# Performance work log

Hardware: AMD Instinct MI355X
Metric: run time of the kernel (lower is better)

Reference implementation:

```python
import jax, jax.numpy as jnp
import numpy as np

N_WIRES = 25                    # odd -> RX on wire 0, then SingleExcitation on (1,2),(3,4),...,(23,24)
DIM = 2 ** N_WIRES              # 33_554_432 amplitudes
N_THETA = (N_WIRES + 1) // 2    # 13


def _apply_rx(state, th, wire):
    """Apply RX(th) = [[cos, -i sin], [-i sin, cos]] (half-angle) to `wire`.
    PennyLane convention: wire 0 is the most-significant bit of the amplitude index."""
    c = jnp.cos(th * 0.5)
    ms = -1j * jnp.sin(th * 0.5)
    st = state.reshape(2 ** wire, 2, -1)          # [pre, 2, post]
    s0, s1 = st[:, 0], st[:, 1]
    new = jnp.stack([c * s0 + ms * s1, ms * s0 + c * s1], axis=1)
    return new.reshape(-1)


def _apply_single_excitation(state, phi, wire):
    """SingleExcitation(phi) on wires [wire, wire+1]: rotates the |01>,|10> subspace
    by angle phi/2; |00>,|11> untouched."""
    c = jnp.cos(phi * 0.5)
    s = jnp.sin(phi * 0.5)
    st = state.reshape(2 ** wire, 2, 2, -1)       # [pre, q_i, q_{i+1}, post]
    a00, a01, a10, a11 = st[:, 0, 0], st[:, 0, 1], st[:, 1, 0], st[:, 1, 1]
    n01 = c * a01 - s * a10
    n10 = s * a01 + c * a10
    new = jnp.stack([jnp.stack([a00, n01], axis=1),
                     jnp.stack([n10, a11], axis=1)], axis=1)
    return new.reshape(-1)


def setup_inputs() -> dict:
    key = jax.random.key(0)
    kf, kt = jax.random.split(key)
    feature = jax.random.normal(kf, (DIM,), dtype=jnp.float32)
    # he_normal init on shape (13, 1): std = sqrt(2 / fan_in) with fan_in = 13
    theta = jax.random.normal(kt, (N_THETA, 1), dtype=jnp.float32) * np.sqrt(2.0 / N_THETA)
    return {"feature": feature, "theta": theta}


def reference(feature, theta) -> jnp.ndarray:
    # AmplitudeEmbedding with pad_with=0.0: pad (no-op here, len == 2^n) then L2-normalize
    state = (feature / jnp.linalg.norm(feature)).astype(jnp.complex64)
    # odd wire count: RX(theta[0][0]) on wire 0, start pair gates at wire 1
    state = _apply_rx(state, theta[0, 0], 0)
    for i in range(1, N_WIRES, 2):                # i = 1,3,...,23 -> theta[0..11]
        state = _apply_single_excitation(state, theta[i // 2, 0], i)
    return jnp.real(state)
```

## Files before the change

### kernel.cpp

```cpp
#include <hip/hip_runtime.h>
#include <math.h>


typedef float f32x4 __attribute__((ext_vector_type(4)));

static __device__ __forceinline__ float4 nt_load4(const float* p) {
    f32x4 v = __builtin_nontemporal_load((const f32x4*)p);
    return *(float4*)&v;
}
static __device__ __forceinline__ void nt_store4(float* p, float4 v) {
    __builtin_nontemporal_store(*(f32x4*)&v, (f32x4*)p);
}

static __device__ __forceinline__ void bar_lgkm() {
    asm volatile("s_waitcnt lgkmcnt(0)\n\ts_barrier" ::: "memory");
}

static __device__ __forceinline__ void rot4(float4& a, float4& b, float c, float s) {
    float4 na, nb;
    na.x = c*a.x - s*b.x;  nb.x = s*a.x + c*b.x;
    na.y = c*a.y - s*b.y;  nb.y = s*a.y + c*b.y;
    na.z = c*a.z - s*b.z;  nb.z = s*a.z + c*b.z;
    na.w = c*a.w - s*b.w;  nb.w = s*a.w + c*b.w;
    a = na; b = nb;
}

static __device__ __forceinline__ float4 shflx4(float4 v, int m) {
    float4 r;
    r.x = __shfl_xor(v.x, m, 64);
    r.y = __shfl_xor(v.y, m, 64);
    r.z = __shfl_xor(v.z, m, 64);
    r.w = __shfl_xor(v.w, m, 64);
    return r;
}

template <int NR>
static __device__ __forceinline__ void rotshfl(float4* f, int sh, float c, float s, int lane) {
    const int pv = (lane >> sh) & 3;
    const bool act = (pv == 1) || (pv == 2);
    const float cl = act ? c : 1.0f;
    const float sl = act ? ((pv == 1) ? -s : s) : 0.0f;
    const int m = 3 << sh;
#pragma unroll
    for (int k = 0; k < NR; ++k) {
        float4 p = shflx4(f[k], m);
        float4 n;
        n.x = fmaf(sl, p.x, cl * f[k].x);
        n.y = fmaf(sl, p.y, cl * f[k].y);
        n.z = fmaf(sl, p.z, cl * f[k].z);
        n.w = fmaf(sl, p.w, cl * f[k].w);
        f[k] = n;
    }
}

static __device__ __forceinline__ float sumsq16(const float4* f) {
    float q[16];
#pragma unroll
    for (int k = 0; k < 16; ++k)
        q[k] = fmaf(f[k].x, f[k].x,
               fmaf(f[k].y, f[k].y,
               fmaf(f[k].z, f[k].z, f[k].w * f[k].w)));
#pragma unroll
    for (int st = 1; st < 16; st <<= 1)
#pragma unroll
        for (int i = 0; i < 16; i += (st << 1))
            q[i] += q[i + st];
    return q[0];
}

__global__ __launch_bounds__(256, 2) void qnn_p1(const float* __restrict__ in,
                                                 const float* __restrict__ theta,
                                                 float* __restrict__ out,
                                                 double* __restrict__ partials) {
    __shared__ __align__(16) float4 lds[4096];
    __shared__ double red[4];
    const int t = threadIdx.x, lane = t & 63, w2 = t >> 6;
    const long gA = (long)blockIdx.x << 13;
    const long gB = gA + 4096;

    float c0,s0,c1,s1,c2,s2,c3,s3,c4,s4,c5,s5,c6,s6;
    { float th;
      th=0.5f*theta[11]; c0=cosf(th); s0=sinf(th);
      th=0.5f*theta[10]; c1=cosf(th); s1=sinf(th);
      th=0.5f*theta[9];  c2=cosf(th); s2=sinf(th);
      th=0.5f*theta[8];  c3=cosf(th); s3=sinf(th);
      th=0.5f*theta[7];  c4=cosf(th); s4=sinf(th);
      th=0.5f*theta[6];  c5=cosf(th); s5=sinf(th);
      th=0.5f*theta[5];  c6=cosf(th); s6=sinf(th); }

    float4 f[16], g[16];
#pragma unroll
    for (int k = 0; k < 16; ++k)
        f[k] = nt_load4(in + ((gA + ((w2 << 10) | (k << 6) | lane)) << 2));
#pragma unroll
    for (int k = 0; k < 16; ++k)
        g[k] = nt_load4(in + ((gB + ((w2 << 10) | (k << 6) | lane)) << 2));

    const float sA = sumsq16(f);

#pragma unroll
    for (int k = 0; k < 16; ++k) {
        float ny = c0*f[k].y - s0*f[k].z;
        float nz = s0*f[k].y + c0*f[k].z;
        f[k].y = ny; f[k].z = nz;
    }
    rotshfl<16>(f, 0, c1, s1, lane);
    rotshfl<16>(f, 2, c2, s2, lane);
    rotshfl<16>(f, 4, c3, s3, lane);
#pragma unroll
    for (int hi = 0; hi < 16; hi += 4) rot4(f[hi+1], f[hi+2], c4, s4);
#pragma unroll
    for (int lo = 0; lo < 4; ++lo)     rot4(f[4+lo], f[8+lo], c5, s5);

#pragma unroll
    for (int k = 0; k < 16; ++k) lds[(w2 << 10) | (k << 6) | lane] = f[k];
    bar_lgkm();
#pragma unroll
    for (int m = 0; m < 16; ++m) f[m] = lds[(m << 8) | (w2 << 6) | lane];
#pragma unroll
    for (int lo = 0; lo < 4; ++lo) rot4(f[4+lo], f[8+lo], c6, s6);
#pragma unroll
    for (int m = 0; m < 16; ++m)
        *(float4*)(out + ((gA + ((m << 8) | (w2 << 6) | lane)) << 2)) = f[m];

    const float sB = sumsq16(g);
#pragma unroll
    for (int k = 0; k < 16; ++k) {
        float ny = c0*g[k].y - s0*g[k].z;
        float nz = s0*g[k].y + c0*g[k].z;
        g[k].y = ny; g[k].z = nz;
    }
    rotshfl<16>(g, 0, c1, s1, lane);
    rotshfl<16>(g, 2, c2, s2, lane);
    rotshfl<16>(g, 4, c3, s3, lane);
#pragma unroll
    for (int hi = 0; hi < 16; hi += 4) rot4(g[hi+1], g[hi+2], c4, s4);
#pragma unroll
    for (int lo = 0; lo < 4; ++lo)     rot4(g[4+lo], g[8+lo], c5, s5);

    bar_lgkm();
#pragma unroll
    for (int k = 0; k < 16; ++k) lds[(w2 << 10) | (k << 6) | lane] = g[k];
    bar_lgkm();
#pragma unroll
    for (int m = 0; m < 16; ++m) g[m] = lds[(m << 8) | (w2 << 6) | lane];
#pragma unroll
    for (int lo = 0; lo < 4; ++lo) rot4(g[4+lo], g[8+lo], c6, s6);
#pragma unroll
    for (int m = 0; m < 16; ++m)
        *(float4*)(out + ((gB + ((m << 8) | (w2 << 6) | lane)) << 2)) = g[m];

    double acc = (double)sA + (double)sB;
#pragma unroll
    for (int off = 32; off > 0; off >>= 1) acc += __shfl_down(acc, off, 64);
    if (lane == 0) red[w2] = acc;
    bar_lgkm();
    if (t == 0)
        partials[blockIdx.x] = red[0] + red[1] + red[2] + red[3];
}

__global__ void qnn_norm(const double* __restrict__ partials,
                         const float* __restrict__ theta,
                         double* __restrict__ scale) {
    __shared__ double w[4];
    const int t = threadIdx.x;
    double acc = 0.0;
    for (int i = t; i < 1024; i += 256) acc += partials[i];
#pragma unroll
    for (int off = 32; off > 0; off >>= 1) acc += __shfl_down(acc, off, 64);
    if ((t & 63) == 0) w[t >> 6] = acc;
    __syncthreads();
    if (t == 0) {
        double tot = w[0] + w[1] + w[2] + w[3];
        *scale = (double)cosf(0.5f * theta[0]) / sqrt(tot);
    }
}

__global__ __launch_bounds__(512, 2) void qnn_high(float* __restrict__ buf,
                                                   const float* __restrict__ theta,
                                                   const double* __restrict__ scale) {
    __shared__ __align__(16) float4 lds[8192];
    const int t = threadIdx.x, lane = t & 63;
    const int bid = blockIdx.x;
    const int b24 = bid >> 8, mid = bid & 255;
    const long baseA = ((long)b24 << 22) | ((long)mid << 4);
    const long baseB = baseA | (1L << 21);

    float c7,s7,c8,s8,c9,s9,c10,s10,c11,s11;
    { float th;
      th=0.5f*theta[4]; c7 =cosf(th); s7 =sinf(th);
      th=0.5f*theta[3]; c8 =cosf(th); s8 =sinf(th);
      th=0.5f*theta[2]; c9 =cosf(th); s9 =sinf(th);
      th=0.5f*theta[1]; c10=cosf(th); s10=sinf(th);
      th=0.5f*theta[0]; c11=cosf(th); s11=sinf(th); }
    const float sc = (float)(*scale);

    float4 f[16], g[16];
#pragma unroll
    for (int k = 0; k < 16; ++k) {
        const int s_ = (k << 9) | t;
        f[k] = *(const float4*)(buf + ((baseA | ((long)(s_ >> 4) << 12) | (s_ & 15)) << 2));
    }
#pragma unroll
    for (int k = 0; k < 16; ++k) {
        const int s_ = (k << 9) | t;
        g[k] = *(const float4*)(buf + ((baseB | ((long)(s_ >> 4) << 12) | (s_ & 15)) << 2));
    }

    rotshfl<16>(f, 4, c7, s7, lane);
    rotshfl<16>(g, 4, c7, s7, lane);
#pragma unroll
    for (int h8 = 0; h8 < 16; h8 += 8) {
        rot4(f[h8+2], f[h8+4], c10, s10);
        rot4(f[h8+3], f[h8+5], c10, s10);
        rot4(g[h8+2], g[h8+4], c10, s10);
        rot4(g[h8+3], g[h8+5], c10, s10);
    }
#pragma unroll
    for (int i = 0; i < 8; ++i)
        rot4(f[8+i], g[i], c11, s11);

#pragma unroll
    for (int k = 0; k < 16; ++k) lds[(k << 9) | t] = f[k];
    bar_lgkm();
    {
        const int rb = ((t >> 6) << 10) | (t & 63);
#pragma unroll
        for (int m = 0; m < 16; ++m) f[m] = lds[rb | (m << 6)];
#pragma unroll
        for (int q = 0; q < 16; q += 4) rot4(f[q+1], f[q+2], c8, s8);
#pragma unroll
        for (int lo = 0; lo < 4; ++lo)  rot4(f[4+lo], f[8+lo], c9, s9);
#pragma unroll
        for (int m = 0; m < 16; ++m) {
            const int s_ = rb | (m << 6);
            float4 v = f[m];
            v.x *= sc; v.y *= sc; v.z *= sc; v.w *= sc;
            nt_store4(buf + ((baseA | ((long)(s_ >> 4) << 12) | (s_ & 15)) << 2), v);
        }
    }
    bar_lgkm();

#pragma unroll
    for (int k = 0; k < 16; ++k) lds[(k << 9) | t] = g[k];
    bar_lgkm();
    {
        const int rb = ((t >> 6) << 10) | (t & 63);
#pragma unroll
        for (int m = 0; m < 16; ++m) g[m] = lds[rb | (m << 6)];
#pragma unroll
        for (int q = 0; q < 16; q += 4) rot4(g[q+1], g[q+2], c8, s8);
#pragma unroll
        for (int lo = 0; lo < 4; ++lo)  rot4(g[4+lo], g[8+lo], c9, s9);
#pragma unroll
        for (int m = 0; m < 16; ++m) {
            const int s_ = rb | (m << 6);
            float4 v = g[m];
            v.x *= sc; v.y *= sc; v.z *= sc; v.w *= sc;
            nt_store4(buf + ((baseB | ((long)(s_ >> 4) << 12) | (s_ & 15)) << 2), v);
        }
    }
}

extern "C" void kernel_launch(void* const* d_in, const int* in_sizes, int n_in,
                              void* d_out, int out_size, void* d_ws, size_t ws_size,
                              hipStream_t stream) {
    const float* in = (const float*)d_in[0];
    const float* theta = (const float*)d_in[1];
    float* out = (float*)d_out;
    double* part = (double*)d_ws;
    double* scale = part + 1024;

    qnn_p1<<<1024, 256, 0, stream>>>(in, theta, out, part);
    qnn_norm<<<1, 256, 0, stream>>>(part, theta, scale);
    qnn_high<<<512, 512, 0, stream>>>(out, theta, scale);
}
```

Baseline: 93.53 us.

## Move theta[4] gate into first pass and rebalance bit-to-pass mapping

Changes which index bits each block of the first pass holds, so the gate on bits 12-13 (theta[4]) is applied there by pairing the A and B tiles, removing the shuffle-based rotation from the second pass. The second pass gets a new address mapping with 32-element contiguous runs in place of 16, so each global access segment is longer. The cost is a data-dependent branch in the first pass and only half the blocks doing the extra rotation, which creates some imbalance between blocks.

```diff
diff --git a/kernel.cpp b/kernel.cpp
--- a/kernel.cpp
+++ b/kernel.cpp
@@ -75,10 +75,12 @@
     __shared__ __align__(16) float4 lds[4096];
     __shared__ double red[4];
     const int t = threadIdx.x, lane = t & 63, w2 = t >> 6;
-    const long gA = (long)blockIdx.x << 13;
-    const long gB = gA + 4096;
-
-    float c0,s0,c1,s1,c2,s2,c3,s3,c4,s4,c5,s5,c6,s6;
+    const int bid = blockIdx.x;
+    const int h = bid >> 1, p = bid & 1;
+    const long gA = ((long)h << 14) | (p ? (1L << 12) : 0);
+    const long gB = ((long)h << 14) | (p ? (2L << 12) : (3L << 12));
+
+    float c0,s0,c1,s1,c2,s2,c3,s3,c4,s4,c5,s5,c6,s6,c7,s7;
     { float th;
       th=0.5f*theta[11]; c0=cosf(th); s0=sinf(th);
       th=0.5f*theta[10]; c1=cosf(th); s1=sinf(th);
@@ -86,7 +88,8 @@
       th=0.5f*theta[8];  c3=cosf(th); s3=sinf(th);
       th=0.5f*theta[7];  c4=cosf(th); s4=sinf(th);
       th=0.5f*theta[6];  c5=cosf(th); s5=sinf(th);
-      th=0.5f*theta[5];  c6=cosf(th); s6=sinf(th); }
+      th=0.5f*theta[5];  c6=cosf(th); s6=sinf(th);
+      th=0.5f*theta[4];  c7=cosf(th); s7=sinf(th); }
 
     float4 f[16], g[16];
 #pragma unroll
@@ -97,6 +100,12 @@
         g[k] = nt_load4(in + ((gB + ((w2 << 10) | (k << 6) | lane)) << 2));
 
     const float sA = sumsq16(f);
+    const float sB = sumsq16(g);
+
+    if (p) {
+#pragma unroll
+        for (int k = 0; k < 16; ++k) rot4(f[k], g[k], c7, s7);
+    }
 
 #pragma unroll
     for (int k = 0; k < 16; ++k) {
@@ -123,7 +132,6 @@
     for (int m = 0; m < 16; ++m)
         *(float4*)(out + ((gA + ((m << 8) | (w2 << 6) | lane)) << 2)) = f[m];
 
-    const float sB = sumsq16(g);
 #pragma unroll
     for (int k = 0; k < 16; ++k) {
         float ny = c0*g[k].y - s0*g[k].z;
@@ -156,7 +164,7 @@
     if (lane == 0) red[w2] = acc;
     bar_lgkm();
     if (t == 0)
-        partials[blockIdx.x] = red[0] + red[1] + red[2] + red[3];
+        partials[bid] = red[0] + red[1] + red[2] + red[3];
 }
 
 __global__ void qnn_norm(const double* __restrict__ partials,
@@ -180,85 +188,78 @@
                                                    const float* __restrict__ theta,
                                                    const double* __restrict__ scale) {
     __shared__ __align__(16) float4 lds[8192];
-    const int t = threadIdx.x, lane = t & 63;
+    const int t = threadIdx.x;
     const int bid = blockIdx.x;
-    const int b24 = bid >> 8, mid = bid & 255;
-    const long baseA = ((long)b24 << 22) | ((long)mid << 4);
-    const long baseB = baseA | (1L << 21);
-
-    float c7,s7,c8,s8,c9,s9,c10,s10,c11,s11;
+    const int f1514 = bid >> 7, mid = bid & 127;
+    const long gqA = ((long)f1514 << 12) | ((long)mid << 5);
+    const long gqB = gqA | (1L << 22);
+
+    float c8,s8,c9,s9,c10,s10,c11,s11;
     { float th;
-      th=0.5f*theta[4]; c7 =cosf(th); s7 =sinf(th);
       th=0.5f*theta[3]; c8 =cosf(th); s8 =sinf(th);
       th=0.5f*theta[2]; c9 =cosf(th); s9 =sinf(th);
       th=0.5f*theta[1]; c10=cosf(th); s10=sinf(th);
       th=0.5f*theta[0]; c11=cosf(th); s11=sinf(th); }
     const float sc = (float)(*scale);
 
+    const int rb = ((t >> 5) << 9) | (t & 31);
+
     float4 f[16], g[16];
 #pragma unroll
     for (int k = 0; k < 16; ++k) {
         const int s_ = (k << 9) | t;
-        f[k] = *(const float4*)(buf + ((baseA | ((long)(s_ >> 4) << 12) | (s_ & 15)) << 2));
+        f[k] = *(const float4*)(buf + ((gqA | ((long)(s_ >> 5) << 14) | (s_ & 31)) << 2));
     }
 #pragma unroll
     for (int k = 0; k < 16; ++k) {
         const int s_ = (k << 9) | t;
-        g[k] = *(const float4*)(buf + ((baseB | ((long)(s_ >> 4) << 12) | (s_ & 15)) << 2));
-    }
-
-    rotshfl<16>(f, 4, c7, s7, lane);
-    rotshfl<16>(g, 4, c7, s7, lane);
-#pragma unroll
-    for (int h8 = 0; h8 < 16; h8 += 8) {
-        rot4(f[h8+2], f[h8+4], c10, s10);
-        rot4(f[h8+3], f[h8+5], c10, s10);
-        rot4(g[h8+2], g[h8+4], c10, s10);
-        rot4(g[h8+3], g[h8+5], c10, s10);
-    }
-#pragma unroll
-    for (int i = 0; i < 8; ++i)
-        rot4(f[8+i], g[i], c11, s11);
+        g[k] = *(const float4*)(buf + ((gqB | ((long)(s_ >> 5) << 14) | (s_ & 31)) << 2));
+    }
+
+#pragma unroll
+    for (int q = 0; q < 16; q += 4) {
+        rot4(f[q+1], f[q+2], c10, s10);
+        rot4(g[q+1], g[q+2], c10, s10);
+    }
+#pragma unroll
+    for (int lo = 0; lo < 4; ++lo) {
+        rot4(f[4+lo], f[8+lo], c11, s11);
+        rot4(g[4+lo], g[8+lo], c11, s11);
+    }
 
 #pragma unroll
     for (int k = 0; k < 16; ++k) lds[(k << 9) | t] = f[k];
     bar_lgkm();
-    {
-        const int rb = ((t >> 6) << 10) | (t & 63);
-#pragma unroll
-        for (int m = 0; m < 16; ++m) f[m] = lds[rb | (m << 6)];
-#pragma unroll
-        for (int q = 0; q < 16; q += 4) rot4(f[q+1], f[q+2], c8, s8);
-#pragma unroll
-        for (int lo = 0; lo < 4; ++lo)  rot4(f[4+lo], f[8+lo], c9, s9);
-#pragma unroll
-        for (int m = 0; m < 16; ++m) {
-            const int s_ = rb | (m << 6);
-            float4 v = f[m];
-            v.x *= sc; v.y *= sc; v.z *= sc; v.w *= sc;
-            nt_store4(buf + ((baseA | ((long)(s_ >> 4) << 12) | (s_ & 15)) << 2), v);
-        }
+#pragma unroll
+    for (int m = 0; m < 16; ++m) f[m] = lds[rb | (m << 5)];
+#pragma unroll
+    for (int q = 0; q < 16; q += 4) rot4(f[q+1], f[q+2], c8, s8);
+#pragma unroll
+    for (int lo = 0; lo < 4; ++lo)  rot4(f[4+lo], f[8+lo], c9, s9);
+#pragma unroll
+    for (int m = 0; m < 16; ++m) {
+        const int s_ = rb | (m << 5);
+        float4 v = f[m];
+        v.x *= sc; v.y *= sc; v.z *= sc; v.w *= sc;
+        nt_store4(buf + ((gqA | ((long)(s_ >> 5) << 14) | (s_ & 31)) << 2), v);
     }
     bar_lgkm();
 
 #pragma unroll
     for (int k = 0; k < 16; ++k) lds[(k << 9) | t] = g[k];
     bar_lgkm();
-    {
-        const int rb = ((t >> 6) << 10) | (t & 63);
-#pragma unroll
-        for (int m = 0; m < 16; ++m) g[m] = lds[rb | (m << 6)];
-#pragma unroll
-        for (int q = 0; q < 16; q += 4) rot4(g[q+1], g[q+2], c8, s8);
-#pragma unroll
-        for (int lo = 0; lo < 4; ++lo)  rot4(g[4+lo], g[8+lo], c9, s9);
-#pragma unroll
-        for (int m = 0; m < 16; ++m) {
-            const int s_ = rb | (m << 6);
-            float4 v = g[m];
-            v.x *= sc; v.y *= sc; v.z *= sc; v.w *= sc;
-            nt_store4(buf + ((baseB | ((long)(s_ >> 4) << 12) | (s_ & 15)) << 2), v);
-        }
+#pragma unroll
+    for (int m = 0; m < 16; ++m) g[m] = lds[rb | (m << 5)];
+#pragma unroll
+    for (int q = 0; q < 16; q += 4) rot4(g[q+1], g[q+2], c8, s8);
+#pragma unroll
+    for (int lo = 0; lo < 4; ++lo)  rot4(g[4+lo], g[8+lo], c9, s9);
+#pragma unroll
+    for (int m = 0; m < 16; ++m) {
+        const int s_ = rb | (m << 5);
+        float4 v = g[m];
+        v.x *= sc; v.y *= sc; v.z *= sc; v.w *= sc;
+        nt_store4(buf + ((gqB | ((long)(s_ >> 5) << 14) | (s_ & 31)) << 2), v);
     }
 }
 
```

New measurement: 116.1 us. 24.2% more time.
